# Kernel tuning notes

Hardware: AMD Instinct MI355X
Metric: run time of the kernel (lower is better)

## Reference

```python
import jax, jax.numpy as jnp
import numpy as np

MARGIN = 0.5
EPS = 1e-8  # torch F.cosine_similarity eps


def setup_inputs() -> dict:
    key = jax.random.key(0)
    k1, k2 = jax.random.split(key)
    N, D = 4096, 1024
    img_emb = jax.random.normal(k1, (N, D), dtype=jnp.float32)
    txt_emb = jax.random.normal(k2, (N, D), dtype=jnp.float32)
    return {"img_emb": img_emb, "txt_emb": txt_emb}


def reference(img_emb, txt_emb):
    N = img_emb.shape[0]
    # norms, clamped at eps exactly like torch cosine_similarity
    img_norm = jnp.maximum(jnp.linalg.norm(img_emb, axis=-1), EPS)  # [N]
    txt_norm = jnp.maximum(jnp.linalg.norm(txt_emb, axis=-1), EPS)  # [N]

    # positive: rowwise cosine similarity
    pos_sim = jnp.sum(img_emb * txt_emb, axis=-1) / (img_norm * txt_norm)  # [N]

    # negative: full pairwise cosine sim as normalized GEMM (avoids N,N,D tensor)
    sim = (img_emb @ txt_emb.T) / (img_norm[:, None] * txt_norm[None, :])  # [N, N]
    sim = sim * (1.0 - jnp.eye(N, dtype=sim.dtype))  # fill_diagonal_(0.0)

    loss_positive = jnp.mean((1.0 - pos_sim) ** 2)
    loss_negative = jnp.mean(jnp.maximum(sim - MARGIN, 0.0) ** 2)
    return loss_positive + loss_negative
```

## Files before the change

### kernel.cpp

```cpp
#include <hip/hip_runtime.h>
#include <hip/hip_bf16.h>

typedef unsigned char  u8;
typedef unsigned int   u32;
typedef __attribute__((ext_vector_type(4))) int   int4v;
typedef __attribute__((ext_vector_type(8))) int   int8v;
typedef __attribute__((ext_vector_type(4))) float float4v;

#define N_ROWS 4096
#define DIM    1024
#define MARGIN 0.5f
#define FP4_SCALE 32.0f
#define INV_SCALE2 (1.0f / (FP4_SCALE * FP4_SCALE))
#define ROWB 512


__device__ __forceinline__ float wave_reduce(float v) {
    #pragma unroll
    for (int off = 32; off > 0; off >>= 1) v += __shfl_xor(v, off, 64);
    return v;
}

__device__ __forceinline__ void gl_lds16(const void* g, void* l) {
    __builtin_amdgcn_global_load_lds(
        (const __attribute__((address_space(1))) void*)g,
        (__attribute__((address_space(3))) void*)l,
        16, 0, 0);
}

__device__ __forceinline__ u32 q4(float v) {
    float a = fabsf(v);
    u32 c = (a >= 0.25f) + (a >= 0.75f) + (a >= 1.25f) + (a >= 1.75f)
          + (a >= 2.5f)  + (a >= 3.5f)  + (a >= 5.0f);
    return c | (v < 0.0f ? 8u : 0u);
}


__global__ __launch_bounds__(256) void rowprep(
        const float* __restrict__ img, const float* __restrict__ txt,
        u8* __restrict__ imgn, u8* __restrict__ txtn,
        float* __restrict__ pospart) {
    const int t = threadIdx.x;
    const int wave = t >> 6, lane = t & 63;
    const int row  = blockIdx.x * 2 + (wave >> 1);
    const int half = wave & 1;

    const float4* ip = (const float4*)img + (size_t)row * 256 + half * 128;
    const float4* tp = (const float4*)txt + (size_t)row * 256 + half * 128;

    float4 iv[2], tv[2];
    #pragma unroll
    for (int k = 0; k < 2; ++k) {
        iv[k] = ip[k * 64 + lane];
        tv[k] = tp[k * 64 + lane];
    }

    float sii = 0.f, si2 = 0.f, st2 = 0.f;
    #pragma unroll
    for (int k = 0; k < 2; ++k) {
        sii += iv[k].x*tv[k].x + iv[k].y*tv[k].y + iv[k].z*tv[k].z + iv[k].w*tv[k].w;
        si2 += iv[k].x*iv[k].x + iv[k].y*iv[k].y + iv[k].z*iv[k].z + iv[k].w*iv[k].w;
        st2 += tv[k].x*tv[k].x + tv[k].y*tv[k].y + tv[k].z*tv[k].z + tv[k].w*tv[k].w;
    }

    sii = wave_reduce(sii);
    si2 = wave_reduce(si2);
    st2 = wave_reduce(st2);

    __shared__ float red[4][3];
    if (lane == 0) { red[wave][0] = sii; red[wave][1] = si2; red[wave][2] = st2; }
    __syncthreads();
    const int pw = wave ^ 1;
    sii += red[pw][0];
    si2 += red[pw][1];
    st2 += red[pw][2];

    float ni = fmaxf(sqrtf(si2), 1e-8f);
    float nt = fmaxf(sqrtf(st2), 1e-8f);
    float ii = 1.0f / ni, it = 1.0f / nt;
    float si = FP4_SCALE * ii, st = FP4_SCALE * it;

    u32 pa = 0, pb = 0;
    #pragma unroll
    for (int k = 0; k < 2; ++k) {
        pa |= q4(iv[k].x * si) << (k*16 + 0);  pa |= q4(iv[k].y * si) << (k*16 + 4);
        pa |= q4(iv[k].z * si) << (k*16 + 8);  pa |= q4(iv[k].w * si) << (k*16 + 12);
        pb |= q4(tv[k].x * st) << (k*16 + 0);  pb |= q4(tv[k].y * st) << (k*16 + 4);
        pb |= q4(tv[k].z * st) << (k*16 + 8);  pb |= q4(tv[k].w * st) << (k*16 + 12);
    }
    ((u32*)imgn)[(size_t)row * 128 + half * 64 + lane] = pa;
    ((u32*)txtn)[(size_t)row * 128 + half * 64 + lane] = pb;

    if (half == 0 && lane == 0) {
        float d = 1.0f - sii * ii * it;
        pospart[row] = d * d;
    }
}


#define BM 128
#define BN 128

__global__ __launch_bounds__(256) void negloss(
        const u8* __restrict__ A, const u8* __restrict__ B,
        float* __restrict__ negpart) {
    __shared__ __align__(16) u8 sA[BM * 128];
    __shared__ __align__(16) u8 sB[BN * 128];

    const int tid = threadIdx.x;
    const int wave = tid >> 6, lane = tid & 63;
    const int wr = wave >> 1, wc = wave & 1;
    const int rA0 = blockIdx.y * BM;
    const int rB0 = blockIdx.x * BN;

    const int mrow = lane & 15;
    const int kg = lane >> 4;

    const int lc = (lane & 7) ^ (lane >> 3);
    const u8* gA0 = A + (size_t)(rA0 + wave * 8 + (lane >> 3)) * ROWB + lc * 16;
    const u8* gB0 = B + (size_t)(rB0 + wave * 8 + (lane >> 3)) * ROWB + lc * 16;

    float4v acc[4][4] = {};

    for (int it = 0; it < 4; ++it) {
        __syncthreads();
        #pragma unroll
        for (int r = 0; r < 4; ++r) {
            int uoff = r * 4096 + wave * 1024;
            gl_lds16(gA0 + (size_t)r * (32 * ROWB) + it * 128, (char*)sA + uoff);
            gl_lds16(gB0 + (size_t)r * (32 * ROWB) + it * 128, (char*)sB + uoff);
        }
        __syncthreads();

        #pragma unroll
        for (int s = 0; s < 2; ++s) {
            const int ch = s * 4 + kg;
            int8v af[4], bf[4];
            #pragma unroll
            for (int i = 0; i < 4; ++i) {
                int ra = wr * 64 + i * 16 + mrow;
                int4v a = *(const int4v*)(sA + ra * 128 + (ch ^ (ra & 7)) * 16);
                int rb = wc * 64 + i * 16 + mrow;
                int4v b = *(const int4v*)(sB + rb * 128 + (ch ^ (rb & 7)) * 16);
                af[i] = int8v{a[0], a[1], a[2], a[3], 0, 0, 0, 0};
                bf[i] = int8v{b[0], b[1], b[2], b[3], 0, 0, 0, 0};
            }
            #pragma unroll
            for (int i = 0; i < 4; ++i)
                #pragma unroll
                for (int j = 0; j < 4; ++j)
                    acc[i][j] = __builtin_amdgcn_mfma_scale_f32_16x16x128_f8f6f4(
                        af[i], bf[j], acc[i][j],
                        4 , 4 ,
                        0, 0x7F7F7F7F ,
                        0, 0x7F7F7F7F );
        }
    }

    float local = 0.0f;
    const int crow = (lane >> 4) * 4;
    const int ccol = lane & 15;
    #pragma unroll
    for (int i = 0; i < 4; ++i) {
        int gi_base = rA0 + wr * 64 + i * 16 + crow;
        #pragma unroll
        for (int j = 0; j < 4; ++j) {
            int gj = rB0 + wc * 64 + j * 16 + ccol;
            #pragma unroll
            for (int r = 0; r < 4; ++r) {
                float sim = acc[i][j][r] * INV_SCALE2;
                float h = fmaxf(sim - MARGIN, 0.0f);
                if (gi_base + r == gj) h = 0.0f;
                local += h * h;
            }
        }
    }

    local = wave_reduce(local);
    __shared__ float part[4];
    if (lane == 0) part[wave] = local;
    __syncthreads();
    if (tid == 0)
        negpart[blockIdx.y * gridDim.x + blockIdx.x] = part[0] + part[1] + part[2] + part[3];
}


__global__ __launch_bounds__(256) void finalize(
        const float* __restrict__ pospart, const float* __restrict__ negpart,
        float* __restrict__ out) {
    const int t = threadIdx.x;
    const int wave = t >> 6, lane = t & 63;
    float sp = 0.f, sn = 0.f;
    #pragma unroll
    for (int i = 0; i < 16; ++i) sp += pospart[i * 256 + t];
    #pragma unroll
    for (int i = 0; i < 4; ++i)  sn += negpart[i * 256 + t];
    sp = wave_reduce(sp);
    sn = wave_reduce(sn);
    __shared__ float rp[4], rn[4];
    if (lane == 0) { rp[wave] = sp; rn[wave] = sn; }
    __syncthreads();
    if (t == 0) {
        float pos = rp[0] + rp[1] + rp[2] + rp[3];
        float neg = rn[0] + rn[1] + rn[2] + rn[3];
        out[0] = pos * (1.0f / (float)N_ROWS)
               + neg * (1.0f / ((float)N_ROWS * (float)N_ROWS));
    }
}


extern "C" void kernel_launch(void* const* d_in, const int* in_sizes, int n_in,
                              void* d_out, int out_size, void* d_ws, size_t ws_size,
                              hipStream_t stream) {
    const float* img = (const float*)d_in[0];
    const float* txt = (const float*)d_in[1];
    float* out = (float*)d_out;

    u8* imgn = (u8*)d_ws;
    u8* txtn = imgn + (size_t)N_ROWS * ROWB;
    float* pospart = (float*)(txtn + (size_t)N_ROWS * ROWB);
    float* negpart = pospart + 4096;

    rowprep<<<N_ROWS / 2, 256, 0, stream>>>(img, txt, imgn, txtn, pospart);
    negloss<<<dim3(N_ROWS / BN, N_ROWS / BM), 256, 0, stream>>>(imgn, txtn, negpart);
    finalize<<<1, 256, 0, stream>>>(pospart, negpart, out);
}
```

Baseline: 89.18 us.

## Double-buffer LDS K-tiles in FP4 GEMM and fuse finalize via last-block ticket

The negloss kernel now splits K into eight 64-byte chunks held in two LDS buffers, prefetching the next chunk while MFMAs consume the current one. This replaces the previous scheme of four loads with two barriers each and no overlap. The separate finalize kernel is removed: each block bumps an atomic ticket that rowprep resets, and the last block to finish does the final reduction, saving one kernel launch. The cost is one extra global atomic per block plus threadfences, and the swizzle now works on 4 chunks instead of 8.

```diff
diff --git a/kernel.cpp b/kernel.cpp
--- a/kernel.cpp
+++ b/kernel.cpp
@@ -14,6 +14,10 @@
 #define INV_SCALE2 (1.0f / (FP4_SCALE * FP4_SCALE))
 #define ROWB 512
 
+#define BM 128
+#define BN 128
+#define NBLK ((N_ROWS / BM) * (N_ROWS / BN))
+
 
 __device__ __forceinline__ float wave_reduce(float v) {
     #pragma unroll
@@ -39,11 +43,13 @@
 __global__ __launch_bounds__(256) void rowprep(
         const float* __restrict__ img, const float* __restrict__ txt,
         u8* __restrict__ imgn, u8* __restrict__ txtn,
-        float* __restrict__ pospart) {
+        float* __restrict__ pospart, u32* __restrict__ ticket) {
     const int t = threadIdx.x;
     const int wave = t >> 6, lane = t & 63;
     const int row  = blockIdx.x * 2 + (wave >> 1);
     const int half = wave & 1;
+
+    if (blockIdx.x == 0 && t == 0) *ticket = 0u;
 
     const float4* ip = (const float4*)img + (size_t)row * 256 + half * 128;
     const float4* tp = (const float4*)txt + (size_t)row * 256 + half * 128;
@@ -98,14 +104,13 @@
 }
 
 
-#define BM 128
-#define BN 128
-
 __global__ __launch_bounds__(256) void negloss(
         const u8* __restrict__ A, const u8* __restrict__ B,
-        float* __restrict__ negpart) {
-    __shared__ __align__(16) u8 sA[BM * 128];
-    __shared__ __align__(16) u8 sB[BN * 128];
+        const float* __restrict__ pospart,
+        float* __restrict__ negpart, u32* __restrict__ ticket,
+        float* __restrict__ out) {
+    __shared__ __align__(16) u8 sA[2][BM * 64];
+    __shared__ __align__(16) u8 sB[2][BN * 64];
 
     const int tid = threadIdx.x;
     const int wave = tid >> 6, lane = tid & 63;
@@ -113,48 +118,58 @@
     const int rA0 = blockIdx.y * BM;
     const int rB0 = blockIdx.x * BN;
 
+    const int lr = lane >> 2;
+    const int lc = (lane & 3) ^ (lr & 3);
+    const u8* gA = A + (size_t)(rA0 + wave * 32 + lr) * ROWB + lc * 16;
+    const u8* gB = B + (size_t)(rB0 + wave * 32 + lr) * ROWB + lc * 16;
+    const int ub = wave * 2048;
+
     const int mrow = lane & 15;
-    const int kg = lane >> 4;
-
-    const int lc = (lane & 7) ^ (lane >> 3);
-    const u8* gA0 = A + (size_t)(rA0 + wave * 8 + (lane >> 3)) * ROWB + lc * 16;
-    const u8* gB0 = B + (size_t)(rB0 + wave * 8 + (lane >> 3)) * ROWB + lc * 16;
+    const int rsw  = ((lane >> 4) ^ (lane & 3)) * 16;
 
     float4v acc[4][4] = {};
 
-    for (int it = 0; it < 4; ++it) {
+    {
+        gl_lds16(gA,            (char*)sA[0] + ub);
+        gl_lds16(gA + 16*ROWB,  (char*)sA[0] + ub + 1024);
+        gl_lds16(gB,            (char*)sB[0] + ub);
+        gl_lds16(gB + 16*ROWB,  (char*)sB[0] + ub + 1024);
+    }
+    __syncthreads();
+
+    int cur = 0;
+    #pragma unroll
+    for (int it = 0; it < 8; ++it) {
+        if (it < 7) {
+            const int nb = cur ^ 1;
+            gl_lds16(gA + (it+1)*64,            (char*)sA[nb] + ub);
+            gl_lds16(gA + 16*ROWB + (it+1)*64,  (char*)sA[nb] + ub + 1024);
+            gl_lds16(gB + (it+1)*64,            (char*)sB[nb] + ub);
+            gl_lds16(gB + 16*ROWB + (it+1)*64,  (char*)sB[nb] + ub + 1024);
+        }
+
+        int8v af[4], bf[4];
+        #pragma unroll
+        for (int i = 0; i < 4; ++i) {
+            int ra = wr * 64 + i * 16 + mrow;
+            int rb = wc * 64 + i * 16 + mrow;
+            int4v a = *(const int4v*)(sA[cur] + ra * 64 + rsw);
+            int4v b = *(const int4v*)(sB[cur] + rb * 64 + rsw);
+            af[i] = int8v{a[0], a[1], a[2], a[3], 0, 0, 0, 0};
+            bf[i] = int8v{b[0], b[1], b[2], b[3], 0, 0, 0, 0};
+        }
+        #pragma unroll
+        for (int i = 0; i < 4; ++i)
+            #pragma unroll
+            for (int j = 0; j < 4; ++j)
+                acc[i][j] = __builtin_amdgcn_mfma_scale_f32_16x16x128_f8f6f4(
+                    af[i], bf[j], acc[i][j],
+                    4 , 4 ,
+                    0, 0x7F7F7F7F ,
+                    0, 0x7F7F7F7F );
+
         __syncthreads();
-        #pragma unroll
-        for (int r = 0; r < 4; ++r) {
-            int uoff = r * 4096 + wave * 1024;
-            gl_lds16(gA0 + (size_t)r * (32 * ROWB) + it * 128, (char*)sA + uoff);
-            gl_lds16(gB0 + (size_t)r * (32 * ROWB) + it * 128, (char*)sB + uoff);
-        }
-        __syncthreads();
-
-        #pragma unroll
-        for (int s = 0; s < 2; ++s) {
-            const int ch = s * 4 + kg;
-            int8v af[4], bf[4];
-            #pragma unroll
-            for (int i = 0; i < 4; ++i) {
-                int ra = wr * 64 + i * 16 + mrow;
-                int4v a = *(const int4v*)(sA + ra * 128 + (ch ^ (ra & 7)) * 16);
-                int rb = wc * 64 + i * 16 + mrow;
-                int4v b = *(const int4v*)(sB + rb * 128 + (ch ^ (rb & 7)) * 16);
-                af[i] = int8v{a[0], a[1], a[2], a[3], 0, 0, 0, 0};
-                bf[i] = int8v{b[0], b[1], b[2], b[3], 0, 0, 0, 0};
-            }
-            #pragma unroll
-            for (int i = 0; i < 4; ++i)
-                #pragma unroll
-                for (int j = 0; j < 4; ++j)
-                    acc[i][j] = __builtin_amdgcn_mfma_scale_f32_16x16x128_f8f6f4(
-                        af[i], bf[j], acc[i][j],
-                        4 , 4 ,
-                        0, 0x7F7F7F7F ,
-                        0, 0x7F7F7F7F );
-        }
+        cur ^= 1;
     }
 
     float local = 0.0f;
@@ -178,29 +193,32 @@
 
     local = wave_reduce(local);
     __shared__ float part[4];
+    __shared__ int lastflag;
     if (lane == 0) part[wave] = local;
     __syncthreads();
-    if (tid == 0)
-        negpart[blockIdx.y * gridDim.x + blockIdx.x] = part[0] + part[1] + part[2] + part[3];
-}
-
-
-__global__ __launch_bounds__(256) void finalize(
-        const float* __restrict__ pospart, const float* __restrict__ negpart,
-        float* __restrict__ out) {
-    const int t = threadIdx.x;
-    const int wave = t >> 6, lane = t & 63;
+    if (tid == 0) {
+        float bsum = part[0] + part[1] + part[2] + part[3];
+        int bid = blockIdx.y * gridDim.x + blockIdx.x;
+        negpart[bid] = bsum;
+        __threadfence();
+        u32 prev = atomicAdd(ticket, 1u);
+        lastflag = (prev == NBLK - 1);
+    }
+    __syncthreads();
+    if (!lastflag) return;
+
+    __threadfence();
     float sp = 0.f, sn = 0.f;
     #pragma unroll
-    for (int i = 0; i < 16; ++i) sp += pospart[i * 256 + t];
-    #pragma unroll
-    for (int i = 0; i < 4; ++i)  sn += negpart[i * 256 + t];
+    for (int i = 0; i < 16; ++i) sp += pospart[i * 256 + tid];
+    #pragma unroll
+    for (int i = 0; i < 4;  ++i) sn += negpart[i * 256 + tid];
     sp = wave_reduce(sp);
     sn = wave_reduce(sn);
     __shared__ float rp[4], rn[4];
     if (lane == 0) { rp[wave] = sp; rn[wave] = sn; }
     __syncthreads();
-    if (t == 0) {
+    if (tid == 0) {
         float pos = rp[0] + rp[1] + rp[2] + rp[3];
         float neg = rn[0] + rn[1] + rn[2] + rn[3];
         out[0] = pos * (1.0f / (float)N_ROWS)
@@ -220,8 +238,9 @@
     u8* txtn = imgn + (size_t)N_ROWS * ROWB;
     float* pospart = (float*)(txtn + (size_t)N_ROWS * ROWB);
     float* negpart = pospart + 4096;
-
-    rowprep<<<N_ROWS / 2, 256, 0, stream>>>(img, txt, imgn, txtn, pospart);
-    negloss<<<dim3(N_ROWS / BN, N_ROWS / BM), 256, 0, stream>>>(imgn, txtn, negpart);
-    finalize<<<1, 256, 0, stream>>>(pospart, negpart, out);
-}
+    u32* ticket = (u32*)(negpart + 1024);
+
+    rowprep<<<N_ROWS / 2, 256, 0, stream>>>(img, txt, imgn, txtn, pospart, ticket);
+    negloss<<<dim3(N_ROWS / BN, N_ROWS / BM), 256, 0, stream>>>(
+        imgn, txtn, pospart, negpart, ticket, out);
+}
```

Result: slower. 108.4 us (+21.5%).
